# Performance work log

Hardware: AMD Instinct MI355X
Metric: run time of the kernel (lower is better)

Reference implementation:

```python
import jax, jax.numpy as jnp
import numpy as np

B, H, N, D, W = 2, 12, 2048, 128, 64  # batch, heads, seq, head_dim (1536/12), nnz per row


def setup_inputs() -> dict:
    key = jax.random.key(0)
    kq, kk, kv, kc = jax.random.split(key, 4)
    q = jax.random.normal(kq, (B, H, N, D), jnp.float32)
    k = jax.random.normal(kk, (B, H, N, D), jnp.float32)
    v = jax.random.normal(kv, (B, H, N, D), jnp.float32)
    # CSR-style sparse attention topology: each query row attends to W columns,
    # column indices sorted within each row (as Sputnik requires).
    col_ids = jnp.sort(jax.random.randint(kc, (N, W), 0, N, dtype=jnp.int32), axis=-1)
    return {"q": q, "k": k, "v": v, "col_ids": col_ids}


def reference(q, k, v, col_ids):
    # SDDMM: scores only at sparse positions -> [B, H, N, W]
    scale = 1.0 / jnp.sqrt(jnp.float32(q.shape[-1]))
    kg = k[:, :, col_ids]  # gather K rows per sparse column: [B, H, N, W, D]
    scores = jnp.einsum('bhnd,bhnwd->bhnw', q, kg) * scale
    # Row-wise sparse softmax (fixed W nnz per row -> dense softmax over last axis)
    probs = jax.nn.softmax(scores, axis=-1)
    # SPMM: sparse probs @ V -> [B, H, N, D]
    vg = v[:, :, col_ids]  # [B, H, N, W, D]
    return jnp.einsum('bhnw,bhnwd->bhnd', probs, vg)
```

## Files before the change

### kernel.cpp

```cpp
#include <hip/hip_runtime.h>
#include <hip/hip_bf16.h>

constexpr int Bc = 2;
constexpr int Hc = 12;
constexpr int Nc = 2048;
constexpr int Dc = 128;
constexpr int Wc = 64;
constexpr float SCALE = 0.08838834764831845f;
constexpr int ELEMS = Bc * Hc * Nc * Dc;

__device__ __forceinline__ float bf_lo(unsigned u) {
    u <<= 16;
    return __builtin_bit_cast(float, u);
}
__device__ __forceinline__ float bf_hi(unsigned u) {
    u &= 0xffff0000u;
    return __builtin_bit_cast(float, u);
}
__device__ __forceinline__ unsigned short f2bf(float f) {
    __hip_bfloat16 h = __float2bfloat16(f);
    return __builtin_bit_cast(unsigned short, h);
}

__global__ __launch_bounds__(256) void cvt_kernel(
    const float* __restrict__ k,
    const float* __restrict__ v,
    unsigned short* __restrict__ kb,
    unsigned short* __restrict__ vb)
{
    const int i = blockIdx.x * 256 + threadIdx.x;
    const float4 kk = ((const float4*)k)[i];
    const float4 vv = ((const float4*)v)[i];
    ushort4 ko, vo;
    ko.x = f2bf(kk.x); ko.y = f2bf(kk.y); ko.z = f2bf(kk.z); ko.w = f2bf(kk.w);
    vo.x = f2bf(vv.x); vo.y = f2bf(vv.y); vo.z = f2bf(vv.z); vo.w = f2bf(vv.w);
    ((ushort4*)kb)[i] = ko;
    ((ushort4*)vb)[i] = vo;
}

__global__ __launch_bounds__(256) void sca_wave_kernel(
    const float* __restrict__ q,
    const unsigned short* __restrict__ kb,
    const unsigned short* __restrict__ vb,
    const int*   __restrict__ col_ids,
    float*       __restrict__ out)
{
    const int t    = threadIdx.x;
    const int wv   = t >> 6;
    const int lane = t & 63;
    const int row  = blockIdx.x * 4 + wv;
    const int n    = row & (Nc - 1);
    const int bh   = row >> 11;

    __shared__ uint2 s_pc[4][Wc];

    const int c_own = col_ids[n * Wc + lane];

    const float*          qrow  = q  + (size_t)row * Dc;
    const unsigned short* kbase = kb + (size_t)bh * Nc * Dc;
    const unsigned short* vbase = vb + (size_t)bh * Nc * Dc;

    const int p  = lane & 3;
    const int qd = lane >> 2;

    float4 qreg[8];
#pragma unroll
    for (int i = 0; i < 4; ++i) {
        qreg[2 * i]     = ((const float4*)qrow)[(p + 4 * i) * 2];
        qreg[2 * i + 1] = ((const float4*)qrow)[(p + 4 * i) * 2 + 1];
    }

    float sc[4];
    int   cs[4];
#pragma unroll
    for (int P = 0; P < 4; ++P) {
        const int w  = P * 16 + qd;
        const int cc = __shfl(c_own, w);
        cs[P] = cc;
        const uint4* krow = (const uint4*)(kbase + (size_t)cc * Dc);
        float acc = 0.0f;
#pragma unroll
        for (int i = 0; i < 4; ++i) {
            const uint4  kk = krow[p + 4 * i];
            const float4 qa = qreg[2 * i];
            const float4 qb = qreg[2 * i + 1];
            acc += bf_lo(kk.x) * qa.x + bf_hi(kk.x) * qa.y
                 + bf_lo(kk.y) * qa.z + bf_hi(kk.y) * qa.w
                 + bf_lo(kk.z) * qb.x + bf_hi(kk.z) * qb.y
                 + bf_lo(kk.w) * qb.z + bf_hi(kk.w) * qb.w;
        }
        acc += __shfl_xor(acc, 1);
        acc += __shfl_xor(acc, 2);
        sc[P] = acc * SCALE;
    }

    float m = fmaxf(fmaxf(sc[0], sc[1]), fmaxf(sc[2], sc[3]));
#pragma unroll
    for (int off = 4; off < 64; off <<= 1) m = fmaxf(m, __shfl_xor(m, off));
    float e0 = __expf(sc[0] - m), e1 = __expf(sc[1] - m);
    float e2 = __expf(sc[2] - m), e3 = __expf(sc[3] - m);
    float s = e0 + e1 + e2 + e3;
#pragma unroll
    for (int off = 4; off < 64; off <<= 1) s += __shfl_xor(s, off);
    const float inv = 1.0f / s;

    if (p == 0) {
        s_pc[wv][qd]      = make_uint2((unsigned)cs[0], __float_as_uint(e0 * inv));
        s_pc[wv][16 + qd] = make_uint2((unsigned)cs[1], __float_as_uint(e1 * inv));
        s_pc[wv][32 + qd] = make_uint2((unsigned)cs[2], __float_as_uint(e2 * inv));
        s_pc[wv][48 + qd] = make_uint2((unsigned)cs[3], __float_as_uint(e3 * inv));
    }
    __builtin_amdgcn_wave_barrier();

    const int g = lane >> 4;
    const int j = lane & 15;
    float4 accA = make_float4(0.f, 0.f, 0.f, 0.f);
    float4 accB = make_float4(0.f, 0.f, 0.f, 0.f);
#pragma unroll
    for (int i = 0; i < 16; ++i) {
        const uint2 pc = s_pc[wv][4 * i + g];
        const float pr = __uint_as_float(pc.y);
        const uint4 vv = ((const uint4*)(vbase + (size_t)pc.x * Dc))[j];
        accA.x += pr * bf_lo(vv.x);
        accA.y += pr * bf_hi(vv.x);
        accA.z += pr * bf_lo(vv.y);
        accA.w += pr * bf_hi(vv.y);
        accB.x += pr * bf_lo(vv.z);
        accB.y += pr * bf_hi(vv.z);
        accB.z += pr * bf_lo(vv.w);
        accB.w += pr * bf_hi(vv.w);
    }
#pragma unroll
    for (int off = 16; off <= 32; off <<= 1) {
        accA.x += __shfl_xor(accA.x, off);
        accA.y += __shfl_xor(accA.y, off);
        accA.z += __shfl_xor(accA.z, off);
        accA.w += __shfl_xor(accA.w, off);
        accB.x += __shfl_xor(accB.x, off);
        accB.y += __shfl_xor(accB.y, off);
        accB.z += __shfl_xor(accB.z, off);
        accB.w += __shfl_xor(accB.w, off);
    }

    if (lane < 16) {
        float4* orow = (float4*)(out + (size_t)row * Dc);
        orow[2 * j]     = accA;
        orow[2 * j + 1] = accB;
    }
}

__global__ __launch_bounds__(256) void sca_kernel(
    const float* __restrict__ q,
    const float* __restrict__ k,
    const float* __restrict__ v,
    const int*   __restrict__ col_ids,
    float*       __restrict__ out)
{
    const int bid = blockIdx.x;
    const int n   = bid & (Nc - 1);
    const int bh  = bid >> 11;
    const int t   = threadIdx.x;

    __shared__ int   s_cols[Wc];
    __shared__ float s_scores[Wc];
    __shared__ float s_probs[Wc];
    __shared__ float s_red[8 * Dc];

    if (t < Wc) s_cols[t] = col_ids[n * Wc + t];

    const float* qrow  = q + ((size_t)bh * Nc + n) * Dc;
    const float* kbase = k + (size_t)bh * Nc * Dc;
    const float* vbase = v + (size_t)bh * Nc * Dc;

    __syncthreads();
    {
        const int w = t >> 2;
        const int p = t & 3;
        const int c = s_cols[w];
        const float4* krow = (const float4*)(kbase + (size_t)c * Dc);
        const float4* q4   = (const float4*)qrow;
        float acc = 0.0f;
#pragma unroll
        for (int i = 0; i < 8; ++i) {
            const float4 kk = krow[p + 4 * i];
            const float4 qq = q4[p + 4 * i];
            acc += kk.x * qq.x + kk.y * qq.y + kk.z * qq.z + kk.w * qq.w;
        }
        acc += __shfl_xor(acc, 1);
        acc += __shfl_xor(acc, 2);
        if (p == 0) s_scores[w] = acc * SCALE;
    }
    __syncthreads();
    if (t < 64) {
        const float sv = s_scores[t];
        float m = sv;
#pragma unroll
        for (int off = 32; off > 0; off >>= 1) m = fmaxf(m, __shfl_xor(m, off));
        const float e = __expf(sv - m);
        float l = e;
#pragma unroll
        for (int off = 32; off > 0; off >>= 1) l += __shfl_xor(l, off);
        s_probs[t] = e / l;
    }
    __syncthreads();
    {
        const int j = t & 31;
        const int g = t >> 5;
        float4 acc = make_float4(0.f, 0.f, 0.f, 0.f);
#pragma unroll
        for (int i = 0; i < 8; ++i) {
            const int w  = g * 8 + i;
            const float pr = s_probs[w];
            const int   c  = s_cols[w];
            const float4 vv = ((const float4*)(vbase + (size_t)c * Dc))[j];
            acc.x += pr * vv.x;
            acc.y += pr * vv.y;
            acc.z += pr * vv.z;
            acc.w += pr * vv.w;
        }
        ((float4*)s_red)[g * 32 + j] = acc;
    }
    __syncthreads();
    if (t < Dc) {
        float sv = 0.0f;
#pragma unroll
        for (int g = 0; g < 8; ++g) sv += s_red[g * Dc + t];
        out[((size_t)bh * Nc + n) * Dc + t] = sv;
    }
}

extern "C" void kernel_launch(void* const* d_in, const int* in_sizes, int n_in,
                              void* d_out, int out_size, void* d_ws, size_t ws_size,
                              hipStream_t stream) {
    const float* q       = (const float*)d_in[0];
    const float* k       = (const float*)d_in[1];
    const float* v       = (const float*)d_in[2];
    const int*   col_ids = (const int*)  d_in[3];
    float*       out     = (float*)d_out;

    const int n_rows = Bc * Hc * Nc;
    const size_t need = (size_t)2 * ELEMS * sizeof(unsigned short);

    if (ws_size >= need) {
        unsigned short* kbp = (unsigned short*)d_ws;
        unsigned short* vbp = kbp + ELEMS;
        cvt_kernel<<<dim3(ELEMS / 4 / 256), dim3(256), 0, stream>>>(k, v, kbp, vbp);
        sca_wave_kernel<<<dim3(n_rows / 4), dim3(256), 0, stream>>>(q, kbp, vbp, col_ids, out);
    } else {
        sca_kernel<<<dim3(n_rows), dim3(256), 0, stream>>>(q, k, v, col_ids, out);
    }
}
```

Baseline: 202.0 us.

## Prefetch V rows before QK scores and pass probabilities via shuffles

The kernel now issues the gathers for the first half of the V rows before the QK dot products, and the second half right after the softmax. The aim is to hide V gather latency behind the score computation. Probabilities and column ids are no longer staged through shared memory; each lane fetches its probability with a cross-lane shuffle from the lane that computed it. The cost is many more live registers for the 16 prefetched uint4 values, which may lower occupancy.

```diff
diff --git a/kernel.cpp b/kernel.cpp
--- a/kernel.cpp
+++ b/kernel.cpp
@@ -52,8 +52,6 @@
     const int n    = row & (Nc - 1);
     const int bh   = row >> 11;
 
-    __shared__ uint2 s_pc[4][Wc];
-
     const int c_own = col_ids[n * Wc + lane];
 
     const float*          qrow  = q  + (size_t)row * Dc;
@@ -62,6 +60,15 @@
 
     const int p  = lane & 3;
     const int qd = lane >> 2;
+    const int g  = lane >> 4;
+    const int j  = lane & 15;
+
+    uint4 vpre[8];
+#pragma unroll
+    for (int i = 0; i < 8; ++i) {
+        const int cc = __shfl(c_own, 4 * i + g);
+        vpre[i] = ((const uint4*)(vbase + (size_t)cc * Dc))[j];
+    }
 
     float4 qreg[8];
 #pragma unroll
@@ -71,12 +78,9 @@
     }
 
     float sc[4];
-    int   cs[4];
 #pragma unroll
     for (int P = 0; P < 4; ++P) {
-        const int w  = P * 16 + qd;
-        const int cc = __shfl(c_own, w);
-        cs[P] = cc;
+        const int cc = __shfl(c_own, P * 16 + qd);
         const uint4* krow = (const uint4*)(kbase + (size_t)cc * Dc);
         float acc = 0.0f;
 #pragma unroll
@@ -97,30 +101,27 @@
     float m = fmaxf(fmaxf(sc[0], sc[1]), fmaxf(sc[2], sc[3]));
 #pragma unroll
     for (int off = 4; off < 64; off <<= 1) m = fmaxf(m, __shfl_xor(m, off));
-    float e0 = __expf(sc[0] - m), e1 = __expf(sc[1] - m);
-    float e2 = __expf(sc[2] - m), e3 = __expf(sc[3] - m);
+    const float e0 = __expf(sc[0] - m), e1 = __expf(sc[1] - m);
+    const float e2 = __expf(sc[2] - m), e3 = __expf(sc[3] - m);
     float s = e0 + e1 + e2 + e3;
 #pragma unroll
     for (int off = 4; off < 64; off <<= 1) s += __shfl_xor(s, off);
     const float inv = 1.0f / s;
-
-    if (p == 0) {
-        s_pc[wv][qd]      = make_uint2((unsigned)cs[0], __float_as_uint(e0 * inv));
-        s_pc[wv][16 + qd] = make_uint2((unsigned)cs[1], __float_as_uint(e1 * inv));
-        s_pc[wv][32 + qd] = make_uint2((unsigned)cs[2], __float_as_uint(e2 * inv));
-        s_pc[wv][48 + qd] = make_uint2((unsigned)cs[3], __float_as_uint(e3 * inv));
-    }
-    __builtin_amdgcn_wave_barrier();
-
-    const int g = lane >> 4;
-    const int j = lane & 15;
+    float pn[4] = { e0 * inv, e1 * inv, e2 * inv, e3 * inv };
+
+    uint4 vnext[8];
+#pragma unroll
+    for (int i = 0; i < 8; ++i) {
+        const int cc = __shfl(c_own, 4 * (i + 8) + g);
+        vnext[i] = ((const uint4*)(vbase + (size_t)cc * Dc))[j];
+    }
+
     float4 accA = make_float4(0.f, 0.f, 0.f, 0.f);
     float4 accB = make_float4(0.f, 0.f, 0.f, 0.f);
 #pragma unroll
     for (int i = 0; i < 16; ++i) {
-        const uint2 pc = s_pc[wv][4 * i + g];
-        const float pr = __uint_as_float(pc.y);
-        const uint4 vv = ((const uint4*)(vbase + (size_t)pc.x * Dc))[j];
+        const uint4 vv = (i < 8) ? vpre[i & 7] : vnext[i & 7];
+        const float pr = __shfl(pn[i >> 2], 16 * (i & 3) + 4 * g);
         accA.x += pr * bf_lo(vv.x);
         accA.y += pr * bf_hi(vv.x);
         accA.z += pr * bf_lo(vv.y);
```

After: 198.9 us. No clear change (-1.6%).
